# Kernel tuning notes

Hardware: AMD Instinct MI355X
Metric: run time of the kernel (lower is better)

The kernel has to match this reference:

```python
import jax, jax.numpy as jnp
import numpy as np

N_SNP, N_GEN, N_PRO = 20000, 5000, 3000
H1, H2, D_OUT = 1024, 256, 1
B = 512


def _mask(key, shape, p=0.05):
    return (jax.random.uniform(key, shape) < p).astype(jnp.float32)


def _linear_params(key, out_dims, in_dims):
    kw, kb = jax.random.split(key)
    bound = 1.0 / np.sqrt(in_dims)
    W = jax.random.uniform(kw, (out_dims, in_dims), minval=-bound, maxval=bound)
    b = jax.random.uniform(kb, (out_dims,), minval=-bound, maxval=bound)
    return W, b


def setup_inputs() -> dict:
    key = jax.random.key(0)
    ks = jax.random.split(key, 12)
    in_mat = jax.random.normal(ks[0], (B, N_PRO + N_GEN + N_SNP), dtype=jnp.float32)
    adj_snp2gen = _mask(ks[1], (N_SNP, N_GEN))
    adj_gen2pro = _mask(ks[2], (N_GEN, N_PRO))
    adj_genpro2pro = _mask(ks[3], (N_GEN + N_PRO, N_PRO))
    adj_pro2pro = _mask(ks[4], (N_PRO, N_PRO))
    W_sg, b_sg = _linear_params(ks[5], N_GEN, N_SNP)
    W_gp, b_gp = _linear_params(ks[6], N_PRO, N_GEN)
    W_br, b_br = _linear_params(ks[7], N_PRO, N_GEN + N_PRO)
    W_pp, b_pp = _linear_params(ks[8], N_PRO, N_PRO)
    W_h1, b_h1 = _linear_params(ks[9], H1, 2 * N_PRO)
    W_h2, b_h2 = _linear_params(ks[10], H2, H1)
    W_out, b_out = _linear_params(ks[11], D_OUT, H2)
    return dict(in_mat=in_mat, adj_snp2gen=adj_snp2gen, adj_gen2pro=adj_gen2pro,
                adj_genpro2pro=adj_genpro2pro, adj_pro2pro=adj_pro2pro,
                W_sg=W_sg, b_sg=b_sg, W_gp=W_gp, b_gp=b_gp,
                W_br=W_br, b_br=b_br, W_pp=W_pp, b_pp=b_pp,
                W_h1=W_h1, b_h1=b_h1, W_h2=W_h2, b_h2=b_h2,
                W_out=W_out, b_out=b_out)


def _omics_layer(x, W, adj, b):
    # x @ (W.T * adj) + b ; W: [out,in], adj: [in,out]
    return x @ (W.T * adj) + b


def reference(in_mat, adj_snp2gen, adj_gen2pro, adj_genpro2pro, adj_pro2pro,
              W_sg, b_sg, W_gp, b_gp, W_br, b_br, W_pp, b_pp,
              W_h1, b_h1, W_h2, b_h2, W_out, b_out):
    snp = in_mat[:, N_PRO + N_GEN:N_PRO + N_GEN + N_SNP]
    gen = in_mat[:, N_PRO:N_PRO + N_GEN]
    pro = in_mat[:, :N_PRO]
    out_snp = jax.nn.relu(_omics_layer(snp, W_sg, adj_snp2gen, b_sg))   # [B, n_gen]
    out_gene = jax.nn.relu(_omics_layer(gen, W_gp, adj_gen2pro, b_gp))  # [B, n_pro]
    in_bridge = jnp.concatenate((out_snp, out_gene), axis=1)            # [B, n_gen+n_pro]
    out_bridge = jax.nn.relu(_omics_layer(in_bridge, W_br, adj_genpro2pro, b_br))
    out_protein = jax.nn.relu(_omics_layer(pro, W_pp, adj_pro2pro, b_pp))
    out_fuse = jnp.concatenate((out_bridge, out_protein), axis=1)       # [B, 2*n_pro]
    # dropout layers are identity (eval mode / drop_rate=0)
    h1 = jax.nn.relu(out_fuse @ W_h1.T + b_h1)
    h2 = jax.nn.relu(h1 @ W_h2.T + b_h2)
    y_pred = jax.nn.sigmoid(h2 @ W_out.T + b_out)
    return y_pred
```

## Files before the change

### kernel.cpp

```cpp
#include <hip/hip_runtime.h>

typedef unsigned short u16;
typedef short bf16x8 __attribute__((ext_vector_type(8)));
typedef float f32x4 __attribute__((ext_vector_type(4)));

#define BM 64
#define BN 64
#define BK 32
#define ADJ_LD 66

__device__ __forceinline__ float bf2f(u16 u) {
    union { unsigned int i; float f; } x;
    x.i = ((unsigned int)u) << 16;
    return x.f;
}
__device__ __forceinline__ u16 f2bf(float f) {
    union { float f; unsigned int i; } x;
    x.f = f;
    unsigned int i = x.i;
    i += 0x7fffu + ((i >> 16) & 1u);
    return (u16)(i >> 16);
}

#define GLOAD16(g, l) __builtin_amdgcn_global_load_lds( \
    (__attribute__((address_space(1))) void*)(g), \
    (__attribute__((address_space(3))) void*)(l), 16, 0, 0)


__global__ __launch_bounds__(256) void convert_a_kernel(
    const float* __restrict__ src, int ld, int srcoff,
    u16* __restrict__ dst, int K, int Kpad, int rows)
{
    const int perrow = Kpad >> 3;
    const int total = rows * perrow;
    for (int idx = blockIdx.x * 256 + threadIdx.x; idx < total; idx += gridDim.x * 256) {
        const int row = idx / perrow;
        const int c8  = (idx - row * perrow) << 3;
        u16 o[8];
        if (c8 + 8 <= K) {
            const float* s = src + (size_t)row * ld + srcoff + c8;
            float4 v0 = *(const float4*)s;
            float4 v1 = *(const float4*)(s + 4);
            o[0] = f2bf(v0.x); o[1] = f2bf(v0.y); o[2] = f2bf(v0.z); o[3] = f2bf(v0.w);
            o[4] = f2bf(v1.x); o[5] = f2bf(v1.y); o[6] = f2bf(v1.z); o[7] = f2bf(v1.w);
        } else {
            #pragma unroll
            for (int q = 0; q < 8; ++q)
                o[q] = (c8 + q < K) ? f2bf(src[(size_t)row * ld + srcoff + c8 + q]) : (u16)0;
        }
        *(uint4*)&dst[(size_t)row * Kpad + c8] = *(const uint4*)o;
    }
}

__global__ __launch_bounds__(256) void mask_weight_kernel(
    const float* __restrict__ W, const float* __restrict__ adj,
    u16* __restrict__ Wm, int N, int K, int Kpad)
{
    __shared__ float adjS[64][65];
    const int t  = threadIdx.x;
    const int k0 = blockIdx.x * 64;
    const int n0 = blockIdx.y * 64;
    const int i0 = t >> 4;
    const int j4 = (t & 15) * 4;

    if (adj) {
        #pragma unroll
        for (int r = 0; r < 4; ++r) {
            const int a  = i0 + 16 * r;
            const int kg = k0 + a;
            float4 v = make_float4(0.f, 0.f, 0.f, 0.f);
            if (kg < K && n0 + j4 < N)
                v = *(const float4*)&adj[(size_t)kg * N + n0 + j4];
            adjS[a][j4 + 0] = v.x; adjS[a][j4 + 1] = v.y;
            adjS[a][j4 + 2] = v.z; adjS[a][j4 + 3] = v.w;
        }
        __syncthreads();
    }
    #pragma unroll
    for (int r = 0; r < 4; ++r) {
        const int i  = i0 + 16 * r;
        const int n  = n0 + i;
        const int kg = k0 + j4;
        float w[4] = {0.f, 0.f, 0.f, 0.f};
        if (n < N && kg < K) {
            const float4 v = *(const float4*)&W[(size_t)n * K + kg];
            w[0] = v.x; w[1] = v.y; w[2] = v.z; w[3] = v.w;
        }
        float m[4] = {1.f, 1.f, 1.f, 1.f};
        if (adj) {
            m[0] = adjS[j4 + 0][i]; m[1] = adjS[j4 + 1][i];
            m[2] = adjS[j4 + 2][i]; m[3] = adjS[j4 + 3][i];
        }
        ushort4 o;
        o.x = f2bf(w[0] * m[0]); o.y = f2bf(w[1] * m[1]);
        o.z = f2bf(w[2] * m[2]); o.w = f2bf(w[3] * m[3]);
        *(ushort4*)&Wm[(size_t)n * Kpad + kg] = o;
    }
}

__global__ void zero_pad_kernel(u16* __restrict__ buf, int ld, int start, int count, int rows)
{
    const int idx = blockIdx.x * blockDim.x + threadIdx.x;
    const int total = rows * count;
    if (idx < total) {
        const int row = idx / count;
        const int c   = idx - row * count;
        buf[(size_t)row * ld + start + c] = 0;
    }
}

__global__ __launch_bounds__(256) void gemm_bf16_kernel(
    const u16* __restrict__ A, int lda,
    const u16* __restrict__ B, int ldb,
    const float* __restrict__ bias,
    u16* __restrict__ C, int ldc, int c_off,
    int N, int Kpad)
{
    __shared__ __align__(16) u16 As[64 * 64];
    __shared__ __align__(16) u16 Bs[64 * 64];

    const int t    = threadIdx.x;
    const int lane = t & 63;
    const int wave = t >> 6;
    const int m0 = blockIdx.y * 64;
    const int n0 = blockIdx.x * 64;

    const int srow = lane >> 3;
    const int scol = (((lane & 7) ^ srow) << 4);

    const char* Ag0 = (const char*)(A + (size_t)(m0 + 16 * wave) * lda);
    const char* Bg0 = (const char*)(B + (size_t)(n0 + 16 * wave) * ldb);
    const size_t lda2 = (size_t)lda * 2, ldb2 = (size_t)ldb * 2;

    char* AsB = (char*)As + 16 * wave * 128 + lane * 16;
    char* BsB = (char*)Bs + 16 * wave * 128 + lane * 16;

    const int wr = wave >> 1, wc = wave & 1;
    const int fr = lane & 15, fq = lane >> 4;
    const int sx = (fr & 7) << 4;

    const char* AsR = (const char*)As + (wr * 32 + fr) * 128;
    const char* BsR = (const char*)Bs + (wc * 32 + fr) * 128;

    f32x4 acc[2][2] = {};
    const int nk = Kpad >> 6;
    for (int kt = 0; kt < nk; ++kt) {
        const size_t kb = (size_t)kt << 7;
        __syncthreads();
        GLOAD16(Ag0 + (size_t)srow * lda2 + kb + scol, AsB);
        GLOAD16(Ag0 + (size_t)(8 + srow) * lda2 + kb + scol, AsB + 1024);
        GLOAD16(Bg0 + (size_t)srow * ldb2 + kb + scol, BsB);
        GLOAD16(Bg0 + (size_t)(8 + srow) * ldb2 + kb + scol, BsB + 1024);
        __syncthreads();
        #pragma unroll
        for (int kk = 0; kk < 2; ++kk) {
            const int ko = (kk * 64 + fq * 16) ^ sx;
            bf16x8 a0 = *(const bf16x8*)(AsR + ko);
            bf16x8 a1 = *(const bf16x8*)(AsR + 16 * 128 + ko);
            bf16x8 b0 = *(const bf16x8*)(BsR + ko);
            bf16x8 b1 = *(const bf16x8*)(BsR + 16 * 128 + ko);
            acc[0][0] = __builtin_amdgcn_mfma_f32_16x16x32_bf16(a0, b0, acc[0][0], 0, 0, 0);
            acc[0][1] = __builtin_amdgcn_mfma_f32_16x16x32_bf16(a0, b1, acc[0][1], 0, 0, 0);
            acc[1][0] = __builtin_amdgcn_mfma_f32_16x16x32_bf16(a1, b0, acc[1][0], 0, 0, 0);
            acc[1][1] = __builtin_amdgcn_mfma_f32_16x16x32_bf16(a1, b1, acc[1][1], 0, 0, 0);
        }
    }

    #pragma unroll
    for (int tn = 0; tn < 2; ++tn) {
        const int gcol = n0 + wc * 32 + tn * 16 + fr;
        if (gcol >= N) continue;
        const float bv = bias[gcol];
        #pragma unroll
        for (int tm = 0; tm < 2; ++tm) {
            #pragma unroll
            for (int r = 0; r < 4; ++r) {
                const int grow = m0 + wr * 32 + tm * 16 + fq * 4 + r;
                float v = acc[tm][tn][r] + bv;
                v = v > 0.f ? v : 0.f;
                C[(size_t)grow * ldc + c_off + gcol] = f2bf(v);
            }
        }
    }
}


__global__ __launch_bounds__(256) void masked_gemm_kernel(
    const void* __restrict__ Av, int lda, int a_off, int a_f32,
    const float* __restrict__ W,
    const float* __restrict__ adj,
    const float* __restrict__ bias,
    u16* __restrict__ C, int ldc, int c_off,
    int N, int K)
{
    __shared__ __align__(16) u16 As[BM * BK];
    __shared__ __align__(16) u16 Bs[BN * BK];
    __shared__ __align__(16) u16 adjS[BK * ADJ_LD];

    const int t  = threadIdx.x;
    const int m0 = blockIdx.y * BM;
    const int n0 = blockIdx.x * BN;

    const int am = t >> 2;
    const int ak = (t & 3) * 8;
    const bool wvalid = (n0 + am) < N;
    const int jk = t >> 3;
    const int jn = (t & 7) * 8;

    const int lane  = t & 63;
    const int wave  = t >> 6;
    const int wm    = (wave >> 1) * 32;
    const int wnoff = (wave & 1) * 32;
    const int fr    = lane & 15;
    const int fq    = lane >> 4;
    const int kq    = fq * 8;

    const float* Af = (const float*)Av + (size_t)(m0 + am) * lda + a_off;
    const u16*   Ah = (const u16*)Av + (size_t)(m0 + am) * lda + a_off;
    const float* Wrow = W + (size_t)(n0 + am) * K;

    f32x4 acc[2][2] = {};

    const int nk = (K + BK - 1) / BK;
    for (int kt = 0; kt < nk; ++kt) {
        const int k0 = kt * BK;
        __syncthreads();
        {
            const int kg = k0 + ak;
            u16* dst = &As[am * BK + ak];
            if (a_f32) {
                if (kg + 8 <= K) {
                    float4 u0 = *(const float4*)&Af[kg];
                    float4 u1 = *(const float4*)&Af[kg + 4];
                    u16 tmp[8] = { f2bf(u0.x), f2bf(u0.y), f2bf(u0.z), f2bf(u0.w),
                                   f2bf(u1.x), f2bf(u1.y), f2bf(u1.z), f2bf(u1.w) };
                    *(uint4*)dst = *(const uint4*)tmp;
                } else {
                    #pragma unroll
                    for (int j = 0; j < 8; ++j)
                        dst[j] = (kg + j < K) ? f2bf(Af[kg + j]) : (u16)0;
                }
            } else {
                if (kg + 8 <= K) {
                    *(uint4*)dst = *(const uint4*)&Ah[kg];
                } else {
                    #pragma unroll
                    for (int j = 0; j < 8; ++j)
                        dst[j] = (kg + j < K) ? Ah[kg + j] : (u16)0;
                }
            }
        }
        {
            const int kg = k0 + ak;
            u16* dst = &Bs[am * BK + ak];
            if (wvalid && kg + 8 <= K) {
                float4 u0 = *(const float4*)&Wrow[kg];
                float4 u1 = *(const float4*)&Wrow[kg + 4];
                u16 tmp[8] = { f2bf(u0.x), f2bf(u0.y), f2bf(u0.z), f2bf(u0.w),
                               f2bf(u1.x), f2bf(u1.y), f2bf(u1.z), f2bf(u1.w) };
                *(uint4*)dst = *(const uint4*)tmp;
            } else {
                #pragma unroll
                for (int j = 0; j < 8; ++j)
                    dst[j] = (wvalid && kg + j < K) ? f2bf(Wrow[kg + j]) : (u16)0;
            }
        }
        if (adj) {
            const int kg = k0 + jk;
            u16* dst = &adjS[jk * ADJ_LD + jn];
            if (kg < K && n0 + jn + 8 <= N) {
                const float* ap = &adj[(size_t)kg * N + n0 + jn];
                float4 u0 = *(const float4*)&ap[0];
                float4 u1 = *(const float4*)&ap[4];
                u16 tmp[8] = { (u16)(u0.x != 0.f), (u16)(u0.y != 0.f),
                               (u16)(u0.z != 0.f), (u16)(u0.w != 0.f),
                               (u16)(u1.x != 0.f), (u16)(u1.y != 0.f),
                               (u16)(u1.z != 0.f), (u16)(u1.w != 0.f) };
                *(uint4*)dst = *(const uint4*)tmp;
            } else {
                #pragma unroll
                for (int j = 0; j < 8; ++j)
                    dst[j] = (kg < K && n0 + jn + j < N)
                                 ? (u16)(adj[(size_t)kg * N + n0 + jn + j] != 0.f) : (u16)0;
            }
            __syncthreads();
            #pragma unroll
            for (int j = 0; j < 8; ++j) {
                if (adjS[(ak + j) * ADJ_LD + am] == 0)
                    Bs[am * BK + ak + j] = 0;
            }
        }
        __syncthreads();

        bf16x8 a0 = *(const bf16x8*)&As[(wm + fr) * BK + kq];
        bf16x8 a1 = *(const bf16x8*)&As[(wm + 16 + fr) * BK + kq];
        bf16x8 b0 = *(const bf16x8*)&Bs[(wnoff + fr) * BK + kq];
        bf16x8 b1 = *(const bf16x8*)&Bs[(wnoff + 16 + fr) * BK + kq];
        acc[0][0] = __builtin_amdgcn_mfma_f32_16x16x32_bf16(a0, b0, acc[0][0], 0, 0, 0);
        acc[0][1] = __builtin_amdgcn_mfma_f32_16x16x32_bf16(a0, b1, acc[0][1], 0, 0, 0);
        acc[1][0] = __builtin_amdgcn_mfma_f32_16x16x32_bf16(a1, b0, acc[1][0], 0, 0, 0);
        acc[1][1] = __builtin_amdgcn_mfma_f32_16x16x32_bf16(a1, b1, acc[1][1], 0, 0, 0);
    }

    #pragma unroll
    for (int tn = 0; tn < 2; ++tn) {
        const int gcol = n0 + wnoff + tn * 16 + fr;
        if (gcol >= N) continue;
        const float bv = bias[gcol];
        #pragma unroll
        for (int tm = 0; tm < 2; ++tm) {
            #pragma unroll
            for (int r = 0; r < 4; ++r) {
                const int grow = m0 + wm + tm * 16 + fq * 4 + r;
                float v = acc[tm][tn][r] + bv;
                v = v > 0.f ? v : 0.f;
                C[(size_t)grow * ldc + c_off + gcol] = f2bf(v);
            }
        }
    }
}

__global__ __launch_bounds__(64) void final_kernel(
    const u16* __restrict__ h2, const float* __restrict__ Wout,
    const float* __restrict__ bout, float* __restrict__ out)
{
    const int r = blockIdx.x;
    const int lane = threadIdx.x;
    float s = 0.f;
    #pragma unroll
    for (int j = 0; j < 4; ++j) {
        const int k = lane * 4 + j;
        s += bf2f(h2[r * 256 + k]) * Wout[k];
    }
    #pragma unroll
    for (int off = 32; off > 0; off >>= 1)
        s += __shfl_down(s, off, 64);
    if (lane == 0) {
        const float x = s + bout[0];
        out[r] = 1.f / (1.f + __expf(-x));
    }
}


extern "C" void kernel_launch(void* const* d_in, const int* in_sizes, int n_in,
                              void* d_out, int out_size, void* d_ws, size_t ws_size,
                              hipStream_t stream) {
    const float* in_mat = (const float*)d_in[0];
    const float* adj_sg = (const float*)d_in[1];
    const float* adj_gp = (const float*)d_in[2];
    const float* adj_br = (const float*)d_in[3];
    const float* adj_pp = (const float*)d_in[4];
    const float* W_sg = (const float*)d_in[5];   const float* b_sg = (const float*)d_in[6];
    const float* W_gp = (const float*)d_in[7];   const float* b_gp = (const float*)d_in[8];
    const float* W_br = (const float*)d_in[9];   const float* b_br = (const float*)d_in[10];
    const float* W_pp = (const float*)d_in[11];  const float* b_pp = (const float*)d_in[12];
    const float* W_h1 = (const float*)d_in[13];  const float* b_h1 = (const float*)d_in[14];
    const float* W_h2 = (const float*)d_in[15];  const float* b_h2 = (const float*)d_in[16];
    const float* W_out = (const float*)d_in[17]; const float* b_out = (const float*)d_in[18];

    const int KP_SG = 20032, KP_GP = 5056, KP_BR = 8000, KP_PP = 3008, KP_H1 = 6016, KP_H2 = 1024;
    const int NP_SG = 5056,  NP_GP = 3008, NP_BR = 3008, NP_PP = 3008, NP_H1 = 1024, NP_H2 = 256;

    u16* p = (u16*)d_ws;
    u16* Asnp = p;  p += (size_t)512 * KP_SG;
    u16* Agen = p;  p += (size_t)512 * KP_GP;
    u16* Apro = p;  p += (size_t)512 * KP_PP;
    u16* Wsg  = p;  p += (size_t)NP_SG * KP_SG;
    u16* Wgp  = p;  p += (size_t)NP_GP * KP_GP;
    u16* Wbr  = p;  p += (size_t)NP_BR * KP_BR;
    u16* Wpp  = p;  p += (size_t)NP_PP * KP_PP;
    u16* Wh1  = p;  p += (size_t)NP_H1 * KP_H1;
    u16* Wh2  = p;  p += (size_t)NP_H2 * KP_H2;
    u16* bridge = p; p += (size_t)512 * 8000;
    u16* fuse   = p; p += (size_t)512 * KP_H1;
    u16* h1c    = p; p += (size_t)512 * 1024;
    u16* h2c    = p; p += (size_t)512 * 256;
    const size_t need_bytes = (size_t)(p - (u16*)d_ws) * 2;

    const dim3 blk(256);
    if (ws_size >= need_bytes) {
        convert_a_kernel<<<dim3(2048), blk, 0, stream>>>(in_mat, 28000, 8000, Asnp, 20000, KP_SG, 512);
        convert_a_kernel<<<dim3(1264), blk, 0, stream>>>(in_mat, 28000, 3000, Agen, 5000, KP_GP, 512);
        convert_a_kernel<<<dim3(752),  blk, 0, stream>>>(in_mat, 28000, 0,    Apro, 3000, KP_PP, 512);
        mask_weight_kernel<<<dim3(KP_SG / 64, NP_SG / 64), blk, 0, stream>>>(W_sg, adj_sg, Wsg, 5000, 20000, KP_SG);
        mask_weight_kernel<<<dim3(KP_GP / 64, NP_GP / 64), blk, 0, stream>>>(W_gp, adj_gp, Wgp, 3000, 5000, KP_GP);
        mask_weight_kernel<<<dim3(KP_BR / 64, NP_BR / 64), blk, 0, stream>>>(W_br, adj_br, Wbr, 3000, 8000, KP_BR);
        mask_weight_kernel<<<dim3(KP_PP / 64, NP_PP / 64), blk, 0, stream>>>(W_pp, adj_pp, Wpp, 3000, 3000, KP_PP);
        mask_weight_kernel<<<dim3(KP_H1 / 64, NP_H1 / 64), blk, 0, stream>>>(W_h1, nullptr, Wh1, 1024, 6000, KP_H1);
        mask_weight_kernel<<<dim3(KP_H2 / 64, NP_H2 / 64), blk, 0, stream>>>(W_h2, nullptr, Wh2, 256, 1024, KP_H2);
        zero_pad_kernel<<<dim3(32), blk, 0, stream>>>(fuse, KP_H1, 6000, 16, 512);

        gemm_bf16_kernel<<<dim3(79, 8), blk, 0, stream>>>(Asnp, KP_SG, Wsg, KP_SG, b_sg, bridge, 8000, 0, 5000, KP_SG);
        gemm_bf16_kernel<<<dim3(47, 8), blk, 0, stream>>>(Agen, KP_GP, Wgp, KP_GP, b_gp, bridge, 8000, 5000, 3000, KP_GP);
        gemm_bf16_kernel<<<dim3(47, 8), blk, 0, stream>>>(bridge, 8000, Wbr, KP_BR, b_br, fuse, KP_H1, 0, 3000, KP_BR);
        gemm_bf16_kernel<<<dim3(47, 8), blk, 0, stream>>>(Apro, KP_PP, Wpp, KP_PP, b_pp, fuse, KP_H1, 3000, 3000, KP_PP);
        gemm_bf16_kernel<<<dim3(16, 8), blk, 0, stream>>>(fuse, KP_H1, Wh1, KP_H1, b_h1, h1c, 1024, 0, 1024, KP_H1);
        gemm_bf16_kernel<<<dim3(4, 8),  blk, 0, stream>>>(h1c, 1024, Wh2, KP_H2, b_h2, h2c, 256, 0, 256, KP_H2);
        final_kernel<<<dim3(512), dim3(64), 0, stream>>>(h2c, W_out, b_out, (float*)d_out);
    } else {
        u16* ws      = (u16*)d_ws;
        u16* bridgeF = ws;
        u16* fuseF   = bridgeF + (size_t)512 * 8000;
        u16* h1F     = fuseF + (size_t)512 * 6000;
        u16* h2F     = h1F + (size_t)512 * 1024;

        masked_gemm_kernel<<<dim3((5000 + 63) / 64, 8), blk, 0, stream>>>(
            in_mat, 28000, 8000, 1, W_sg, adj_sg, b_sg, bridgeF, 8000, 0, 5000, 20000);
        masked_gemm_kernel<<<dim3((3000 + 63) / 64, 8), blk, 0, stream>>>(
            in_mat, 28000, 3000, 1, W_gp, adj_gp, b_gp, bridgeF, 8000, 5000, 3000, 5000);
        masked_gemm_kernel<<<dim3((3000 + 63) / 64, 8), blk, 0, stream>>>(
            bridgeF, 8000, 0, 0, W_br, adj_br, b_br, fuseF, 6000, 0, 3000, 8000);
        masked_gemm_kernel<<<dim3((3000 + 63) / 64, 8), blk, 0, stream>>>(
            in_mat, 28000, 0, 1, W_pp, adj_pp, b_pp, fuseF, 6000, 3000, 3000, 3000);
        masked_gemm_kernel<<<dim3(1024 / 64, 8), blk, 0, stream>>>(
            fuseF, 6000, 0, 0, W_h1, nullptr, b_h1, h1F, 1024, 0, 1024, 6000);
        masked_gemm_kernel<<<dim3(256 / 64, 8), blk, 0, stream>>>(
            h1F, 1024, 0, 0, W_h2, nullptr, b_h2, h2F, 256, 0, 256, 1024);
        final_kernel<<<dim3(512), dim3(64), 0, stream>>>(h2F, W_out, b_out, (float*)d_out);
    }
}
```

Baseline: 1.712 ms.

## Batch prep kernels, group independent GEMMs, and triple-buffer GEMM k-loop

Merges the ten preprocessing launches (activation conversion, weight masking, zero padding) into one task-indexed prep kernel. Launches the three independent first-layer GEMMs as one grouped kernel. Replaces the sync-load-sync loop in the bf16 GEMM with a three-stage LDS ring that prefetches two tiles ahead and uses explicit vmcnt waits. The aim is less launch overhead, better CU fill, and global-load latency hidden behind MFMA work, at the cost of three times the LDS per block and fragile hand-coded waitcnt logic.

New measurement: 1.612 ms. 1.06x faster.

```diff
diff --git a/kernel.cpp b/kernel.cpp
--- a/kernel.cpp
+++ b/kernel.cpp
@@ -3,11 +3,6 @@
 typedef unsigned short u16;
 typedef short bf16x8 __attribute__((ext_vector_type(8)));
 typedef float f32x4 __attribute__((ext_vector_type(4)));
-
-#define BM 64
-#define BN 64
-#define BK 32
-#define ADJ_LD 66
 
 __device__ __forceinline__ float bf2f(u16 u) {
     union { unsigned int i; float f; } x;
@@ -27,131 +22,165 @@
     (__attribute__((address_space(3))) void*)(l), 16, 0, 0)
 
 
-__global__ __launch_bounds__(256) void convert_a_kernel(
-    const float* __restrict__ src, int ld, int srcoff,
-    u16* __restrict__ dst, int K, int Kpad, int rows)
-{
-    const int perrow = Kpad >> 3;
-    const int total = rows * perrow;
-    for (int idx = blockIdx.x * 256 + threadIdx.x; idx < total; idx += gridDim.x * 256) {
-        const int row = idx / perrow;
-        const int c8  = (idx - row * perrow) << 3;
-        u16 o[8];
-        if (c8 + 8 <= K) {
-            const float* s = src + (size_t)row * ld + srcoff + c8;
-            float4 v0 = *(const float4*)s;
-            float4 v1 = *(const float4*)(s + 4);
-            o[0] = f2bf(v0.x); o[1] = f2bf(v0.y); o[2] = f2bf(v0.z); o[3] = f2bf(v0.w);
-            o[4] = f2bf(v1.x); o[5] = f2bf(v1.y); o[6] = f2bf(v1.z); o[7] = f2bf(v1.w);
-        } else {
-            #pragma unroll
-            for (int q = 0; q < 8; ++q)
-                o[q] = (c8 + q < K) ? f2bf(src[(size_t)row * ld + srcoff + c8 + q]) : (u16)0;
-        }
-        *(uint4*)&dst[(size_t)row * Kpad + c8] = *(const uint4*)o;
-    }
-}
-
-__global__ __launch_bounds__(256) void mask_weight_kernel(
-    const float* __restrict__ W, const float* __restrict__ adj,
-    u16* __restrict__ Wm, int N, int K, int Kpad)
+struct PrepTask {
+    int type;
+    const float* a;
+    const float* b;
+    u16* dst;
+    int N, K, Kpad, ld, off, base, cnt;
+};
+struct PrepBatch { PrepTask t[10]; int ntask; };
+
+__global__ __launch_bounds__(256) void prep_kernel(PrepBatch pb)
 {
     __shared__ float adjS[64][65];
-    const int t  = threadIdx.x;
-    const int k0 = blockIdx.x * 64;
-    const int n0 = blockIdx.y * 64;
-    const int i0 = t >> 4;
-    const int j4 = (t & 15) * 4;
-
-    if (adj) {
+    const int bid = blockIdx.x;
+    int ti = 0;
+    #pragma unroll
+    for (int i = 1; i < 10; ++i)
+        if (i < pb.ntask && bid >= pb.t[i].base) ti = i;
+    const PrepTask tk = pb.t[ti];
+    const int local = bid - tk.base;
+    const int t = threadIdx.x;
+
+    if (tk.type == 0) {
+        const int nx = tk.Kpad >> 6;
+        const int k0 = (local % nx) * 64;
+        const int n0 = (local / nx) * 64;
+        const int i0 = t >> 4;
+        const int j4 = (t & 15) * 4;
+        if (tk.b) {
+            #pragma unroll
+            for (int r = 0; r < 4; ++r) {
+                const int a  = i0 + 16 * r;
+                const int kg = k0 + a;
+                float4 v = make_float4(0.f, 0.f, 0.f, 0.f);
+                if (kg < tk.K && n0 + j4 < tk.N)
+                    v = *(const float4*)&tk.b[(size_t)kg * tk.N + n0 + j4];
+                adjS[a][j4 + 0] = v.x; adjS[a][j4 + 1] = v.y;
+                adjS[a][j4 + 2] = v.z; adjS[a][j4 + 3] = v.w;
+            }
+            __syncthreads();
+        }
         #pragma unroll
         for (int r = 0; r < 4; ++r) {
-            const int a  = i0 + 16 * r;
-            const int kg = k0 + a;
-            float4 v = make_float4(0.f, 0.f, 0.f, 0.f);
-            if (kg < K && n0 + j4 < N)
-                v = *(const float4*)&adj[(size_t)kg * N + n0 + j4];
-            adjS[a][j4 + 0] = v.x; adjS[a][j4 + 1] = v.y;
-            adjS[a][j4 + 2] = v.z; adjS[a][j4 + 3] = v.w;
-        }
-        __syncthreads();
-    }
-    #pragma unroll
-    for (int r = 0; r < 4; ++r) {
-        const int i  = i0 + 16 * r;
-        const int n  = n0 + i;
-        const int kg = k0 + j4;
-        float w[4] = {0.f, 0.f, 0.f, 0.f};
-        if (n < N && kg < K) {
-            const float4 v = *(const float4*)&W[(size_t)n * K + kg];
-            w[0] = v.x; w[1] = v.y; w[2] = v.z; w[3] = v.w;
-        }
-        float m[4] = {1.f, 1.f, 1.f, 1.f};
-        if (adj) {
-            m[0] = adjS[j4 + 0][i]; m[1] = adjS[j4 + 1][i];
-            m[2] = adjS[j4 + 2][i]; m[3] = adjS[j4 + 3][i];
-        }
-        ushort4 o;
-        o.x = f2bf(w[0] * m[0]); o.y = f2bf(w[1] * m[1]);
-        o.z = f2bf(w[2] * m[2]); o.w = f2bf(w[3] * m[3]);
-        *(ushort4*)&Wm[(size_t)n * Kpad + kg] = o;
-    }
-}
-
-__global__ void zero_pad_kernel(u16* __restrict__ buf, int ld, int start, int count, int rows)
+            const int i  = i0 + 16 * r;
+            const int n  = n0 + i;
+            const int kg = k0 + j4;
+            float w[4] = {0.f, 0.f, 0.f, 0.f};
+            if (n < tk.N && kg < tk.K) {
+                const float4 v = *(const float4*)&tk.a[(size_t)n * tk.K + kg];
+                w[0] = v.x; w[1] = v.y; w[2] = v.z; w[3] = v.w;
+            }
+            float m[4] = {1.f, 1.f, 1.f, 1.f};
+            if (tk.b) {
+                m[0] = adjS[j4 + 0][i]; m[1] = adjS[j4 + 1][i];
+                m[2] = adjS[j4 + 2][i]; m[3] = adjS[j4 + 3][i];
+            }
+            ushort4 o;
+            o.x = f2bf(w[0] * m[0]); o.y = f2bf(w[1] * m[1]);
+            o.z = f2bf(w[2] * m[2]); o.w = f2bf(w[3] * m[3]);
+            *(ushort4*)&tk.dst[(size_t)n * tk.Kpad + kg] = o;
+        }
+    } else if (tk.type == 1) {
+        const int perrow = tk.Kpad >> 3;
+        const int total = 512 * perrow;
+        for (int idx = local * 256 + t; idx < total; idx += tk.cnt * 256) {
+            const int row = idx / perrow;
+            const int c8  = (idx - row * perrow) << 3;
+            u16 o[8];
+            if (c8 + 8 <= tk.K) {
+                const float* s = tk.a + (size_t)row * tk.ld + tk.off + c8;
+                float4 v0 = *(const float4*)s;
+                float4 v1 = *(const float4*)(s + 4);
+                o[0] = f2bf(v0.x); o[1] = f2bf(v0.y); o[2] = f2bf(v0.z); o[3] = f2bf(v0.w);
+                o[4] = f2bf(v1.x); o[5] = f2bf(v1.y); o[6] = f2bf(v1.z); o[7] = f2bf(v1.w);
+            } else {
+                #pragma unroll
+                for (int q = 0; q < 8; ++q)
+                    o[q] = (c8 + q < tk.K) ? f2bf(tk.a[(size_t)row * tk.ld + tk.off + c8 + q]) : (u16)0;
+            }
+            *(uint4*)&tk.dst[(size_t)row * tk.Kpad + c8] = *(const uint4*)o;
+        }
+    } else {
+        const int idx = local * 256 + t;
+        const int total = 512 * tk.K;
+        if (idx < total) {
+            const int row = idx / tk.K;
+            const int c   = idx - row * tk.K;
+            tk.dst[(size_t)row * tk.ld + tk.off + c] = 0;
+        }
+    }
+}
+
+
+struct GemmTask {
+    const u16* A; const u16* B; const float* bias; u16* C;
+    int lda, ldb, ldc, c_off, N, nk, base;
+};
+struct GemmBatch { GemmTask t[3]; int ntask; };
+
+__global__ __launch_bounds__(256) void gemm_bf16_kernel(GemmBatch gb)
 {
-    const int idx = blockIdx.x * blockDim.x + threadIdx.x;
-    const int total = rows * count;
-    if (idx < total) {
-        const int row = idx / count;
-        const int c   = idx - row * count;
-        buf[(size_t)row * ld + start + c] = 0;
-    }
-}
-
-__global__ __launch_bounds__(256) void gemm_bf16_kernel(
-    const u16* __restrict__ A, int lda,
-    const u16* __restrict__ B, int ldb,
-    const float* __restrict__ bias,
-    u16* __restrict__ C, int ldc, int c_off,
-    int N, int Kpad)
-{
-    __shared__ __align__(16) u16 As[64 * 64];
-    __shared__ __align__(16) u16 Bs[64 * 64];
+    __shared__ __align__(16) u16 As[3][64 * 64];
+    __shared__ __align__(16) u16 Bs[3][64 * 64];
 
     const int t    = threadIdx.x;
     const int lane = t & 63;
     const int wave = t >> 6;
-    const int m0 = blockIdx.y * 64;
-    const int n0 = blockIdx.x * 64;
+
+    int ti = 0;
+    if (gb.ntask > 1 && (int)blockIdx.x >= gb.t[1].base) ti = 1;
+    if (gb.ntask > 2 && (int)blockIdx.x >= gb.t[2].base) ti = 2;
+    const GemmTask tk = gb.t[ti];
+    const int local = (int)blockIdx.x - tk.base;
+    const int m0 = (local & 7) * 64;
+    const int n0 = (local >> 3) * 64;
 
     const int srow = lane >> 3;
     const int scol = (((lane & 7) ^ srow) << 4);
 
-    const char* Ag0 = (const char*)(A + (size_t)(m0 + 16 * wave) * lda);
-    const char* Bg0 = (const char*)(B + (size_t)(n0 + 16 * wave) * ldb);
-    const size_t lda2 = (size_t)lda * 2, ldb2 = (size_t)ldb * 2;
-
-    char* AsB = (char*)As + 16 * wave * 128 + lane * 16;
-    char* BsB = (char*)Bs + 16 * wave * 128 + lane * 16;
+    const char* Ag0 = (const char*)(tk.A + (size_t)(m0 + 16 * wave) * tk.lda);
+    const char* Bg0 = (const char*)(tk.B + (size_t)(n0 + 16 * wave) * tk.ldb);
+    const size_t lda2 = (size_t)tk.lda * 2, ldb2 = (size_t)tk.ldb * 2;
+    const size_t aoff0 = (size_t)srow * lda2 + scol;
+    const size_t aoff1 = (size_t)(8 + srow) * lda2 + scol;
+    const size_t boff0 = (size_t)srow * ldb2 + scol;
+    const size_t boff1 = (size_t)(8 + srow) * ldb2 + scol;
+    const int sb = 16 * wave * 128 + lane * 16;
 
     const int wr = wave >> 1, wc = wave & 1;
     const int fr = lane & 15, fq = lane >> 4;
     const int sx = (fr & 7) << 4;
-
-    const char* AsR = (const char*)As + (wr * 32 + fr) * 128;
-    const char* BsR = (const char*)Bs + (wc * 32 + fr) * 128;
+    const int rA = (wr * 32 + fr) * 128;
+    const int rB = (wc * 32 + fr) * 128;
 
     f32x4 acc[2][2] = {};
-    const int nk = Kpad >> 6;
+    const int nk = tk.nk;
+
+#define STAGE(tt, bb) do { \
+        const size_t kb = (size_t)(tt) << 7; \
+        GLOAD16(Ag0 + kb + aoff0, (char*)As[bb] + sb); \
+        GLOAD16(Ag0 + kb + aoff1, (char*)As[bb] + sb + 1024); \
+        GLOAD16(Bg0 + kb + boff0, (char*)Bs[bb] + sb); \
+        GLOAD16(Bg0 + kb + boff1, (char*)Bs[bb] + sb + 1024); \
+    } while (0)
+
+    STAGE(0, 0);
+    if (nk > 1) STAGE(1, 1);
+
     for (int kt = 0; kt < nk; ++kt) {
-        const size_t kb = (size_t)kt << 7;
-        __syncthreads();
-        GLOAD16(Ag0 + (size_t)srow * lda2 + kb + scol, AsB);
-        GLOAD16(Ag0 + (size_t)(8 + srow) * lda2 + kb + scol, AsB + 1024);
-        GLOAD16(Bg0 + (size_t)srow * ldb2 + kb + scol, BsB);
-        GLOAD16(Bg0 + (size_t)(8 + srow) * ldb2 + kb + scol, BsB + 1024);
-        __syncthreads();
+        const int cb = kt % 3;
+        if (kt + 2 < nk) STAGE(kt + 2, (kt + 2) % 3);
+        const int ahead = nk - 1 - kt;
+        if (ahead >= 2)      asm volatile("s_waitcnt vmcnt(8)" ::: "memory");
+        else if (ahead == 1) asm volatile("s_waitcnt vmcnt(4)" ::: "memory");
+        else                 asm volatile("s_waitcnt vmcnt(0)" ::: "memory");
+        __builtin_amdgcn_sched_barrier(0);
+        __builtin_amdgcn_s_barrier();
+
+        const char* AsR = (const char*)As[cb] + rA;
+        const char* BsR = (const char*)Bs[cb] + rB;
         #pragma unroll
         for (int kk = 0; kk < 2; ++kk) {
             const int ko = (kk * 64 + fq * 16) ^ sx;
@@ -164,13 +193,15 @@
             acc[1][0] = __builtin_amdgcn_mfma_f32_16x16x32_bf16(a1, b0, acc[1][0], 0, 0, 0);
             acc[1][1] = __builtin_amdgcn_mfma_f32_16x16x32_bf16(a1, b1, acc[1][1], 0, 0, 0);
         }
-    }
+        __builtin_amdgcn_s_barrier();
+    }
+#undef STAGE
 
     #pragma unroll
     for (int tn = 0; tn < 2; ++tn) {
         const int gcol = n0 + wc * 32 + tn * 16 + fr;
-        if (gcol >= N) continue;
-        const float bv = bias[gcol];
+        if (gcol >= tk.N) continue;
+        const float bv = tk.bias[gcol];
         #pragma unroll
         for (int tm = 0; tm < 2; ++tm) {
             #pragma unroll
@@ -178,12 +209,39 @@
                 const int grow = m0 + wr * 32 + tm * 16 + fq * 4 + r;
                 float v = acc[tm][tn][r] + bv;
                 v = v > 0.f ? v : 0.f;
-                C[(size_t)grow * ldc + c_off + gcol] = f2bf(v);
-            }
-        }
-    }
-}
-
+                tk.C[(size_t)grow * tk.ldc + tk.c_off + gcol] = f2bf(v);
+            }
+        }
+    }
+}
+
+
+__global__ __launch_bounds__(64) void final_kernel(
+    const u16* __restrict__ h2, const float* __restrict__ Wout,
+    const float* __restrict__ bout, float* __restrict__ out)
+{
+    const int r = blockIdx.x;
+    const int lane = threadIdx.x;
+    float s = 0.f;
+    #pragma unroll
+    for (int j = 0; j < 4; ++j) {
+        const int k = lane * 4 + j;
+        s += bf2f(h2[r * 256 + k]) * Wout[k];
+    }
+    #pragma unroll
+    for (int off = 32; off > 0; off >>= 1)
+        s += __shfl_down(s, off, 64);
+    if (lane == 0) {
+        const float x = s + bout[0];
+        out[r] = 1.f / (1.f + __expf(-x));
+    }
+}
+
+
+#define BM 64
+#define BN 64
+#define BK 32
+#define ADJ_LD 66
 
 __global__ __launch_bounds__(256) void masked_gemm_kernel(
     const void* __restrict__ Av, int lda, int a_off, int a_f32,
@@ -320,27 +378,6 @@
     }
 }
 
-__global__ __launch_bounds__(64) void final_kernel(
-    const u16* __restrict__ h2, const float* __restrict__ Wout,
-    const float* __restrict__ bout, float* __restrict__ out)
-{
-    const int r = blockIdx.x;
-    const int lane = threadIdx.x;
-    float s = 0.f;
-    #pragma unroll
-    for (int j = 0; j < 4; ++j) {
-        const int k = lane * 4 + j;
-        s += bf2f(h2[r * 256 + k]) * Wout[k];
-    }
-    #pragma unroll
-    for (int off = 32; off > 0; off >>= 1)
-        s += __shfl_down(s, off, 64);
-    if (lane == 0) {
-        const float x = s + bout[0];
-        out[r] = 1.f / (1.f + __expf(-x));
-    }
-}
-
 
 extern "C" void kernel_launch(void* const* d_in, const int* in_sizes, int n_in,
                               void* d_out, int out_size, void* d_ws, size_t ws_size,
@@ -379,23 +416,52 @@
 
     const dim3 blk(256);
     if (ws_size >= need_bytes) {
-        convert_a_kernel<<<dim3(2048), blk, 0, stream>>>(in_mat, 28000, 8000, Asnp, 20000, KP_SG, 512);
-        convert_a_kernel<<<dim3(1264), blk, 0, stream>>>(in_mat, 28000, 3000, Agen, 5000, KP_GP, 512);
-        convert_a_kernel<<<dim3(752),  blk, 0, stream>>>(in_mat, 28000, 0,    Apro, 3000, KP_PP, 512);
-        mask_weight_kernel<<<dim3(KP_SG / 64, NP_SG / 64), blk, 0, stream>>>(W_sg, adj_sg, Wsg, 5000, 20000, KP_SG);
-        mask_weight_kernel<<<dim3(KP_GP / 64, NP_GP / 64), blk, 0, stream>>>(W_gp, adj_gp, Wgp, 3000, 5000, KP_GP);
-        mask_weight_kernel<<<dim3(KP_BR / 64, NP_BR / 64), blk, 0, stream>>>(W_br, adj_br, Wbr, 3000, 8000, KP_BR);
-        mask_weight_kernel<<<dim3(KP_PP / 64, NP_PP / 64), blk, 0, stream>>>(W_pp, adj_pp, Wpp, 3000, 3000, KP_PP);
-        mask_weight_kernel<<<dim3(KP_H1 / 64, NP_H1 / 64), blk, 0, stream>>>(W_h1, nullptr, Wh1, 1024, 6000, KP_H1);
-        mask_weight_kernel<<<dim3(KP_H2 / 64, NP_H2 / 64), blk, 0, stream>>>(W_h2, nullptr, Wh2, 256, 1024, KP_H2);
-        zero_pad_kernel<<<dim3(32), blk, 0, stream>>>(fuse, KP_H1, 6000, 16, 512);
-
-        gemm_bf16_kernel<<<dim3(79, 8), blk, 0, stream>>>(Asnp, KP_SG, Wsg, KP_SG, b_sg, bridge, 8000, 0, 5000, KP_SG);
-        gemm_bf16_kernel<<<dim3(47, 8), blk, 0, stream>>>(Agen, KP_GP, Wgp, KP_GP, b_gp, bridge, 8000, 5000, 3000, KP_GP);
-        gemm_bf16_kernel<<<dim3(47, 8), blk, 0, stream>>>(bridge, 8000, Wbr, KP_BR, b_br, fuse, KP_H1, 0, 3000, KP_BR);
-        gemm_bf16_kernel<<<dim3(47, 8), blk, 0, stream>>>(Apro, KP_PP, Wpp, KP_PP, b_pp, fuse, KP_H1, 3000, 3000, KP_PP);
-        gemm_bf16_kernel<<<dim3(16, 8), blk, 0, stream>>>(fuse, KP_H1, Wh1, KP_H1, b_h1, h1c, 1024, 0, 1024, KP_H1);
-        gemm_bf16_kernel<<<dim3(4, 8),  blk, 0, stream>>>(h1c, 1024, Wh2, KP_H2, b_h2, h2c, 256, 0, 256, KP_H2);
+        PrepBatch pb{};
+        int base = 0;
+        auto addm = [&](const float* W, const float* adj, u16* dst, int N, int K, int Kp, int Np) {
+            int cnt = (Kp / 64) * (Np / 64);
+            pb.t[pb.ntask++] = PrepTask{0, W, adj, dst, N, K, Kp, 0, 0, base, cnt};
+            base += cnt;
+        };
+        auto addc = [&](int off, u16* dst, int K, int Kp, int cnt) {
+            pb.t[pb.ntask++] = PrepTask{1, in_mat, nullptr, dst, 0, K, Kp, 28000, off, base, cnt};
+            base += cnt;
+        };
+        addm(W_sg, adj_sg, Wsg, 5000, 20000, KP_SG, NP_SG);
+        addm(W_br, adj_br, Wbr, 3000, 8000,  KP_BR, NP_BR);
+        addm(W_gp, adj_gp, Wgp, 3000, 5000,  KP_GP, NP_GP);
+        addm(W_pp, adj_pp, Wpp, 3000, 3000,  KP_PP, NP_PP);
+        addm(W_h1, nullptr, Wh1, 1024, 6000, KP_H1, NP_H1);
+        addm(W_h2, nullptr, Wh2, 256, 1024,  KP_H2, NP_H2);
+        addc(8000, Asnp, 20000, KP_SG, 1024);
+        addc(3000, Agen, 5000,  KP_GP, 320);
+        addc(0,    Apro, 3000,  KP_PP, 192);
+        pb.t[pb.ntask++] = PrepTask{2, nullptr, nullptr, fuse, 0, 16, 0, KP_H1, 6000, base, 32};
+        base += 32;
+        prep_kernel<<<dim3(base), blk, 0, stream>>>(pb);
+
+        GemmBatch g1{};
+        g1.t[0] = GemmTask{Asnp, Wsg, b_sg, bridge, KP_SG, KP_SG, 8000, 0,    5000, KP_SG / 64, 0};
+        g1.t[1] = GemmTask{Agen, Wgp, b_gp, bridge, KP_GP, KP_GP, 8000, 5000, 3000, KP_GP / 64, 632};
+        g1.t[2] = GemmTask{Apro, Wpp, b_pp, fuse,   KP_PP, KP_PP, KP_H1, 3000, 3000, KP_PP / 64, 1008};
+        g1.ntask = 3;
+        gemm_bf16_kernel<<<dim3(1384), blk, 0, stream>>>(g1);
+
+        GemmBatch g2{};
+        g2.t[0] = GemmTask{bridge, Wbr, b_br, fuse, 8000, KP_BR, KP_H1, 0, 3000, KP_BR / 64, 0};
+        g2.ntask = 1;
+        gemm_bf16_kernel<<<dim3(376), blk, 0, stream>>>(g2);
+
+        GemmBatch g3{};
+        g3.t[0] = GemmTask{fuse, Wh1, b_h1, h1c, KP_H1, KP_H1, 1024, 0, 1024, KP_H1 / 64, 0};
+        g3.ntask = 1;
+        gemm_bf16_kernel<<<dim3(128), blk, 0, stream>>>(g3);
+
+        GemmBatch g4{};
+        g4.t[0] = GemmTask{h1c, Wh2, b_h2, h2c, KP_H2, KP_H2, 256, 0, 256, KP_H2 / 64, 0};
+        g4.ntask = 1;
+        gemm_bf16_kernel<<<dim3(32), blk, 0, stream>>>(g4);
+
         final_kernel<<<dim3(512), dim3(64), 0, stream>>>(h2c, W_out, b_out, (float*)d_out);
     } else {
         u16* ws      = (u16*)d_ws;
```
